# Performance work log

Measured on AMD Instinct MI355X. Metric: run time of the kernel, lower is better.

The kernel has to match this reference:

```python
import jax, jax.numpy as jnp
import numpy as np

N = 129  # fixed by fc1: 3*121 -> N-8 = 121
F = 262144
E = 16384

def setup_inputs() -> dict:
    key = jax.random.key(0)
    ks = jax.random.split(key, 18)
    s = 0.05
    return {
        "x": jax.random.normal(ks[0], (N, F), jnp.float32),
        "edge_index": jax.random.randint(ks[1], (2, E), 0, N),
        "edge_attr": jax.random.uniform(ks[2], (E, 3), jnp.float32),
        # GCNConvSortPool (channel1 only; forward reuses it for all 3 edge channels)
        "gcn1_W": jax.random.normal(ks[3], (F, 1), jnp.float32) * (1.0 / np.sqrt(F)),
        "gcn1_b": jnp.zeros((1,), jnp.float32),
        "gcn2_W": jax.random.normal(ks[4], (1, 1), jnp.float32),
        "gcn2_b": jnp.zeros((1,), jnp.float32),
        "conv1_w": jax.random.normal(ks[5], (3, 2, 3), jnp.float32) * s,  # OIH
        "conv1_b": jax.random.normal(ks[6], (3,), jnp.float32) * s,
        "conv2_w": jax.random.normal(ks[7], (1, 3, 3), jnp.float32) * s,
        "conv2_b": jax.random.normal(ks[8], (1,), jnp.float32) * s,
        "fc1_W": jax.random.normal(ks[9], (3 * 121, 32), jnp.float32) * s,
        "fc1_b": jnp.zeros((32,), jnp.float32),
        "fc2_W": jax.random.normal(ks[10], (32, 6), jnp.float32) * s,
        "fc2_b": jnp.zeros((6,), jnp.float32),
        "fc3_W": jax.random.normal(ks[11], (6, 2), jnp.float32) * s,
        "fc3_b": jnp.zeros((2,), jnp.float32),
    }

def _gcn_conv(x, row, col, ew, W, b):
    # PyG GCNConv with edge weights: add self loops (weight 1), symmetric norm.
    n = x.shape[0]
    xw = x @ W                                             # [n, out]
    loop = jnp.arange(n)
    row2 = jnp.concatenate([row, loop])
    col2 = jnp.concatenate([col, loop])
    ew2 = jnp.concatenate([ew, jnp.ones((n,), x.dtype)])
    deg = jax.ops.segment_sum(ew2, col2, num_segments=n)
    dinv = jnp.where(deg > 0, deg ** -0.5, 0.0)
    norm = dinv[row2] * ew2 * dinv[col2]                   # [e+n]
    out = jax.ops.segment_sum(norm[:, None] * xw[row2], col2, num_segments=n)
    return out + b

def _maxpool1d3(z):
    return jax.lax.reduce_window(z, -jnp.inf, jax.lax.max, (1, 1, 3), (1, 1, 1), 'VALID')

def _conv1d(z, w, b):
    out = jax.lax.conv_general_dilated(z, w, (1,), 'VALID', dimension_numbers=('NCH', 'OIH', 'NCH'))
    return out + b[None, :, None]

def _channel(x, row, col, ew, gcn1_W, gcn1_b, gcn2_W, gcn2_b, conv1_w, conv1_b, conv2_w, conv2_b):
    h1 = _gcn_conv(x, row, col, ew, gcn1_W, gcn1_b)        # [N,1]
    h2 = _gcn_conv(h1[:, -1:], row, col, ew, gcn2_W, gcn2_b)  # [N,1]
    h = jnp.concatenate([h1, h2], axis=-1)                 # [N,2]
    perm = jnp.argsort(-h[:, -1])                          # SortPool: sort by last channel, descending, k=N
    h = h[perm]                                            # [N,2]
    z = h.T[None]                                          # [1,2,N]
    z = _maxpool1d3(_conv1d(z, conv1_w, conv1_b))          # [1,3,N-4]
    z = _maxpool1d3(_conv1d(z, conv2_w, conv2_b))          # [1,1,N-8]
    return z

def reference(x, edge_index, edge_attr, gcn1_W, gcn1_b, gcn2_W, gcn2_b,
              conv1_w, conv1_b, conv2_w, conv2_b,
              fc1_W, fc1_b, fc2_W, fc2_b, fc3_W, fc3_b):
    row, col = edge_index[0], edge_index[1]
    outs = [_channel(x, row, col, edge_attr[:, c], gcn1_W, gcn1_b, gcn2_W, gcn2_b,
                     conv1_w, conv1_b, conv2_w, conv2_b) for c in range(3)]
    all_x = jnp.concatenate(outs, axis=-2)                 # [1,3,121]
    h = all_x.reshape(1, -1)                               # [1,363]
    h = jax.nn.elu(h @ fc1_W + fc1_b)                      # dropout=0 -> identity
    h = jax.nn.elu(h @ fc2_W + fc2_b)
    return h @ fc3_W + fc3_b                               # [1,2]
```

## Files before the change

kernel.cpp:

```cpp
#include <hip/hip_runtime.h>
#include <hip/hip_bf16.h>
#include <math.h>

#define NN 129
#define FF 262144
#define EE 16384
#define CHUNKS 32
#define CHUNK (FF / CHUNKS)
#define NMV (NN * CHUNKS)

#define EPT_T (EE / 256)
#define BATCH 8
#define NBATCH (EPT_T / BATCH)

#define OFF_PARTIAL 0
#define OFF_BAR     (OFF_PARTIAL + NMV)
#define OFF_SORT    (OFF_BAR + 1024)
#define LSTRIDE 32

typedef float vfloat4 __attribute__((ext_vector_type(4)));

__global__ __launch_bounds__(256) void k_fused(
    const float* __restrict__ x, const float* __restrict__ W,
    const int* __restrict__ eidx, const float* __restrict__ eattr,
    double* __restrict__ ws,
    const float* __restrict__ b1, const float* __restrict__ W2, const float* __restrict__ b2,
    const float* __restrict__ c1w, const float* __restrict__ c1b,
    const float* __restrict__ c2w, const float* __restrict__ c2b,
    const float* __restrict__ f1W, const float* __restrict__ f1b,
    const float* __restrict__ f2W, const float* __restrict__ f2b,
    const float* __restrict__ f3W, const float* __restrict__ f3b,
    float* __restrict__ out)
{
    const int b = blockIdx.x;
    const int tid = threadIdx.x;
    const int wave = tid >> 6, lane = tid & 63;

    __shared__ double P[129 + 387 + 387];
    __shared__ double SCR[1935];
    __shared__ int    sbin[NN];
    __shared__ int    scur[NN];
    __shared__ double ws4[4];
    __shared__ double fcb[38];

    unsigned* sync = (unsigned*)(ws + OFF_BAR);

    if (b != 0) {
        const int bm = b - 1;
        const int r = bm / CHUNKS, ch = bm % CHUNKS;
        const vfloat4* xp = (const vfloat4*)(x + (size_t)r * FF + (size_t)ch * CHUNK);
        const float4*  wp = (const float4*)(W + (size_t)ch * CHUNK);
        double acc0 = 0.0, acc1 = 0.0;
#pragma unroll
        for (int i = 0; i < CHUNK / (256 * 4); ++i) {
            vfloat4 xv = __builtin_nontemporal_load(xp + tid + i * 256);
            float4  wv = wp[tid + i * 256];
            acc0 += (double)xv[0] * (double)wv.x + (double)xv[1] * (double)wv.y;
            acc1 += (double)xv[2] * (double)wv.z + (double)xv[3] * (double)wv.w;
        }
        double acc = acc0 + acc1;
        for (int off = 32; off > 0; off >>= 1) acc += __shfl_down(acc, off, 64);
        if (lane == 0) ws4[wave] = acc;
        __syncthreads();
        if (tid == 0) {
            const double v = (ws4[0] + ws4[1]) + (ws4[2] + ws4[3]);
            __hip_atomic_store(&ws[OFF_PARTIAL + bm], v,
                               __ATOMIC_RELAXED, __HIP_MEMORY_SCOPE_AGENT);
            asm volatile("s_waitcnt vmcnt(0)" ::: "memory");
            __hip_atomic_fetch_add(&sync[(bm & 63) * LSTRIDE], 1u,
                                   __ATOMIC_RELAXED, __HIP_MEMORY_SCOPE_AGENT);
        }
        return;
    }

    double* sxw   = P;
    double* sdinv = P + 129;
    double* sh1   = P + 516;
    double* agg   = SCR;
    float4* recs  = (float4*)(ws + OFF_SORT);

    for (int i = tid; i < NN; i += 256) sbin[i] = 0;
    __syncthreads();
    for (int bt = 0; bt < NBATCH; ++bt) {
        int c8[BATCH];
#pragma unroll
        for (int i = 0; i < BATCH; ++i)
            c8[i] = eidx[EE + (bt * BATCH + i) * 256 + tid];
#pragma unroll
        for (int i = 0; i < BATCH; ++i) atomicAdd(&sbin[c8[i]], 1);
    }
    __syncthreads();
    if (tid == 0) {
        int run = 0;
        for (int j = 0; j < NN; ++j) { scur[j] = run; run += sbin[j]; }
    }
    __syncthreads();
    for (int bt = 0; bt < NBATCH; ++bt) {
        int r8[BATCH], c8[BATCH];
        float a8[BATCH][3];
#pragma unroll
        for (int i = 0; i < BATCH; ++i) {
            const int e = (bt * BATCH + i) * 256 + tid;
            r8[i] = eidx[e];
            c8[i] = eidx[EE + e];
            a8[i][0] = eattr[e * 3 + 0];
            a8[i][1] = eattr[e * 3 + 1];
            a8[i][2] = eattr[e * 3 + 2];
        }
#pragma unroll
        for (int i = 0; i < BATCH; ++i) {
            const int pos = atomicAdd(&scur[c8[i]], 1);
            float4 rec;
            rec.x = __int_as_float((r8[i] << 8) | c8[i]);
            rec.y = a8[i][0]; rec.z = a8[i][1]; rec.w = a8[i][2];
            recs[pos] = rec;
        }
    }
    __threadfence_block();
    __syncthreads();

    for (int i = tid; i < 3 * NN; i += 256) agg[i] = 0.0;
    __syncthreads();
    {
        const int base = tid * EPT_T;
        double a0 = 0.0, a1 = 0.0, a2 = 0.0;
        int cur = -1;
#pragma unroll 4
        for (int k = 0; k < EPT_T; ++k) {
            const float4 rec = recs[base + k];
            const int rc = __float_as_int(rec.x);
            const int cl = rc & 255;
            if (cl != cur) {
                if (cur >= 0) {
                    unsafeAtomicAdd(&agg[0 * NN + cur], a0);
                    unsafeAtomicAdd(&agg[1 * NN + cur], a1);
                    unsafeAtomicAdd(&agg[2 * NN + cur], a2);
                }
                cur = cl; a0 = a1 = a2 = 0.0;
            }
            a0 += (double)rec.y; a1 += (double)rec.z; a2 += (double)rec.w;
        }
        if (cur >= 0) {
            unsafeAtomicAdd(&agg[0 * NN + cur], a0);
            unsafeAtomicAdd(&agg[1 * NN + cur], a1);
            unsafeAtomicAdd(&agg[2 * NN + cur], a2);
        }
    }
    __syncthreads();
    for (int v = tid; v < 3 * NN; v += 256) {
        const double d = 1.0 + agg[v];
        sdinv[v] = (d > 0.0) ? 1.0 / sqrt(d) : 0.0;
    }
    __syncthreads();

    if (tid < 64) {
        unsigned* c = sync + tid * LSTRIDE;
        const unsigned expct = (tid < 32) ? 65u : 64u;
        while (__hip_atomic_load(c, __ATOMIC_RELAXED, __HIP_MEMORY_SCOPE_AGENT) < expct)
            __builtin_amdgcn_s_sleep(8);
    }
    __syncthreads();

    for (int j = tid; j < NN; j += 256) {
        double s = 0.0;
#pragma unroll
        for (int k = 0; k < CHUNKS; ++k)
            s += __hip_atomic_load(&ws[OFF_PARTIAL + j * CHUNKS + k],
                                   __ATOMIC_RELAXED, __HIP_MEMORY_SCOPE_AGENT);
        sxw[j] = s;
    }
    for (int i = tid; i < 3 * NN; i += 256) agg[i] = 0.0;
    __syncthreads();

    {
        const int base = tid * EPT_T;
        double a0 = 0.0, a1 = 0.0, a2 = 0.0;
        int cur = -1;
#pragma unroll 4
        for (int k = 0; k < EPT_T; ++k) {
            const float4 rec = recs[base + k];
            const int rc = __float_as_int(rec.x);
            const int cl = rc & 255, r = rc >> 8;
            if (cl != cur) {
                if (cur >= 0) {
                    unsafeAtomicAdd(&agg[0 * NN + cur], a0);
                    unsafeAtomicAdd(&agg[1 * NN + cur], a1);
                    unsafeAtomicAdd(&agg[2 * NN + cur], a2);
                }
                cur = cl; a0 = a1 = a2 = 0.0;
            }
            const double xwr = sxw[r];
            const double nw0 = sdinv[0 * NN + r] * (double)rec.y * sdinv[0 * NN + cl];
            const double nw1 = sdinv[1 * NN + r] * (double)rec.z * sdinv[1 * NN + cl];
            const double nw2 = sdinv[2 * NN + r] * (double)rec.w * sdinv[2 * NN + cl];
            a0 += nw0 * xwr; a1 += nw1 * xwr; a2 += nw2 * xwr;
        }
        if (cur >= 0) {
            unsafeAtomicAdd(&agg[0 * NN + cur], a0);
            unsafeAtomicAdd(&agg[1 * NN + cur], a1);
            unsafeAtomicAdd(&agg[2 * NN + cur], a2);
        }
    }
    __syncthreads();

    const double bb1 = (double)b1[0];
    for (int i = tid; i < 3 * NN; i += 256) {
        const int j = i % NN;
        const double dv = sdinv[i];
        sh1[i] = dv * dv * sxw[j] + bb1 + agg[i];
    }
    __syncthreads();
    for (int i = tid; i < 3 * NN; i += 256) agg[i] = 0.0;
    __syncthreads();

    const double w2 = (double)W2[0];
    {
        const int base = tid * EPT_T;
        double a0 = 0.0, a1 = 0.0, a2 = 0.0;
        int cur = -1;
#pragma unroll 4
        for (int k = 0; k < EPT_T; ++k) {
            const float4 rec = recs[base + k];
            const int rc = __float_as_int(rec.x);
            const int cl = rc & 255, r = rc >> 8;
            if (cl != cur) {
                if (cur >= 0) {
                    unsafeAtomicAdd(&agg[0 * NN + cur], a0);
                    unsafeAtomicAdd(&agg[1 * NN + cur], a1);
                    unsafeAtomicAdd(&agg[2 * NN + cur], a2);
                }
                cur = cl; a0 = a1 = a2 = 0.0;
            }
            const double nw0 = sdinv[0 * NN + r] * (double)rec.y * sdinv[0 * NN + cl];
            const double nw1 = sdinv[1 * NN + r] * (double)rec.z * sdinv[1 * NN + cl];
            const double nw2 = sdinv[2 * NN + r] * (double)rec.w * sdinv[2 * NN + cl];
            a0 += nw0 * (sh1[0 * NN + r] * w2);
            a1 += nw1 * (sh1[1 * NN + r] * w2);
            a2 += nw2 * (sh1[2 * NN + r] * w2);
        }
        if (cur >= 0) {
            unsafeAtomicAdd(&agg[0 * NN + cur], a0);
            unsafeAtomicAdd(&agg[1 * NN + cur], a1);
            unsafeAtomicAdd(&agg[2 * NN + cur], a2);
        }
    }
    __syncthreads();

    double* h2f = SCR + 1548;
    const double bb2 = (double)b2[0];
    for (int i = tid; i < 3 * NN; i += 256) {
        const int j = i % NN; (void)j;
        const double dv = sdinv[i];
        h2f[i] = dv * dv * (sh1[i] * w2) + bb2 + agg[i];
    }
    __syncthreads();

    double* z0   = SCR;
    double* z1   = SCR + 387;
    int*    rnk  = (int*)(SCR + 774);
    double* c1o  = SCR + 774;
    double* c2o  = SCR;
    double* allx = SCR + 369;
    double* fc1o = fcb;
    double* fc2o = fcb + 32;

    for (int i = tid; i < 3 * NN; i += 256) {
        const int c = i / NN, j = i % NN;
        const double v = h2f[c * NN + j];
        int rk = 0;
        for (int q = 0; q < NN; ++q) {
            const double u = h2f[c * NN + q];
            rk += (u > v) || (u == v && q < j);
        }
        rnk[i] = rk;
    }
    __syncthreads();
    for (int i = tid; i < 3 * NN; i += 256) {
        const int c = i / NN;
        const int rk = rnk[i];
        z0[c * NN + rk] = sh1[i];
        z1[c * NN + rk] = h2f[i];
    }
    __syncthreads();

    for (int i = tid; i < 3 * 3 * 127; i += 256) {
        const int c = i / (3 * 127), rem = i % (3 * 127), o = rem / 127, p = rem % 127;
        double s = (double)c1b[o];
#pragma unroll
        for (int k = 0; k < 3; ++k) {
            s += (double)c1w[(o * 2 + 0) * 3 + k] * z0[c * NN + p + k];
            s += (double)c1w[(o * 2 + 1) * 3 + k] * z1[c * NN + p + k];
        }
        c1o[(c * 3 + o) * 127 + p] = s;
    }
    __syncthreads();

    for (int i = tid; i < 3 * 123; i += 256) {
        const int c = i / 123, p = i % 123;
        double s = (double)c2b[0];
#pragma unroll
        for (int ic = 0; ic < 3; ++ic)
#pragma unroll
            for (int k = 0; k < 3; ++k) {
                const double* base = c1o + (c * 3 + ic) * 127 + p + k;
                const double m = fmax(base[0], fmax(base[1], base[2]));
                s += (double)c2w[ic * 3 + k] * m;
            }
        c2o[c * 123 + p] = s;
    }
    __syncthreads();
    for (int i = tid; i < 3 * 121; i += 256) {
        const int c = i / 121, p = i % 121;
        allx[c * 121 + p] = fmax(c2o[c * 123 + p],
                            fmax(c2o[c * 123 + p + 1], c2o[c * 123 + p + 2]));
    }
    __syncthreads();

    {
        const int j = tid >> 3, t = tid & 7;
        double s = 0.0;
        for (int i = t; i < 363; i += 8) s += allx[i] * (double)f1W[i * 32 + j];
        s += __shfl_down(s, 4, 8);
        s += __shfl_down(s, 2, 8);
        s += __shfl_down(s, 1, 8);
        if (t == 0) {
            s += (double)f1b[j];
            fc1o[j] = (s > 0.0) ? s : expm1(s);
        }
    }
    __syncthreads();
    if (tid < 6) {
        double s = (double)f2b[tid];
        for (int i = 0; i < 32; ++i) s += fc1o[i] * (double)f2W[i * 6 + tid];
        fc2o[tid] = (s > 0.0) ? s : expm1(s);
    }
    __syncthreads();
    if (tid < 2) {
        double s = (double)f3b[tid];
        for (int i = 0; i < 6; ++i) s += fc2o[i] * (double)f3W[i * 2 + tid];
        out[tid] = (float)s;
    }
}

extern "C" void kernel_launch(void* const* d_in, const int* in_sizes, int n_in,
                              void* d_out, int out_size, void* d_ws, size_t ws_size,
                              hipStream_t stream) {
    const float* x    = (const float*)d_in[0];
    const int*   eidx = (const int*)d_in[1];
    const float* eattr= (const float*)d_in[2];
    const float* g1W  = (const float*)d_in[3];
    const float* g1b  = (const float*)d_in[4];
    const float* g2W  = (const float*)d_in[5];
    const float* g2b  = (const float*)d_in[6];
    const float* c1w  = (const float*)d_in[7];
    const float* c1b  = (const float*)d_in[8];
    const float* c2w  = (const float*)d_in[9];
    const float* c2b  = (const float*)d_in[10];
    const float* f1W  = (const float*)d_in[11];
    const float* f1b  = (const float*)d_in[12];
    const float* f2W  = (const float*)d_in[13];
    const float* f2b  = (const float*)d_in[14];
    const float* f3W  = (const float*)d_in[15];
    const float* f3b  = (const float*)d_in[16];
    float* out = (float*)d_out;
    double* ws = (double*)d_ws;

    hipMemsetAsync((void*)(ws + OFF_BAR), 0, 64 * 128, stream);
    k_fused<<<NMV + 1, 256, 0, stream>>>(
        x, g1W, eidx, eattr, ws,
        g1b, g2W, g2b, c1w, c1b, c2w, c2b,
        f1W, f1b, f2W, f2b, f3W, f3b, out);
}
```

Before: 303.8 us.

## Drop per-launch memset by self-resetting device-global sync counters; batch edge scans

Replaces the workspace-based barrier counters, which were zeroed by a hipMemsetAsync before every launch, with a __device__ global array that block 0 resets to zero at the end of the kernel. This removes one extra GPU operation per call. The three edge-scan loops are factored into a templated helper that loads 8 records at a time, the partial-sum gather is batched, the scatter batch shrinks from 8 to 4, and launch bounds now request 6 blocks per SM. Correctness across calls now depends on every launch finishing its reset; an aborted run would leave stale counters.

```diff
diff --git a/kernel.cpp b/kernel.cpp
--- a/kernel.cpp
+++ b/kernel.cpp
@@ -1,5 +1,4 @@
 #include <hip/hip_runtime.h>
-#include <hip/hip_bf16.h>
 #include <math.h>
 
 #define NN 129
@@ -10,17 +9,74 @@
 #define NMV (NN * CHUNKS)
 
 #define EPT_T (EE / 256)
-#define BATCH 8
-#define NBATCH (EPT_T / BATCH)
+#define SB 8
+#define NSB (EPT_T / SB)
 
 #define OFF_PARTIAL 0
-#define OFF_BAR     (OFF_PARTIAL + NMV)
-#define OFF_SORT    (OFF_BAR + 1024)
+#define OFF_SORT    (OFF_PARTIAL + NMV)
+
 #define LSTRIDE 32
+__device__ __align__(128) unsigned g_sync[64 * LSTRIDE];
 
 typedef float vfloat4 __attribute__((ext_vector_type(4)));
 
-__global__ __launch_bounds__(256) void k_fused(
+__device__ __forceinline__ double agent_ld(const double* p) {
+    return __hip_atomic_load(p, __ATOMIC_RELAXED, __HIP_MEMORY_SCOPE_AGENT);
+}
+__device__ __forceinline__ void agent_st(double* p, double v) {
+    __hip_atomic_store(p, v, __ATOMIC_RELAXED, __HIP_MEMORY_SCOPE_AGENT);
+}
+
+template<int MODE>
+__device__ __forceinline__ void scan_edges(
+    const float4* __restrict__ recs, double* agg,
+    const double* sdinv, const double* sxw, const double* sh1,
+    double w2, int tid)
+{
+    const int base = tid * EPT_T;
+    double a0 = 0.0, a1 = 0.0, a2 = 0.0;
+    int cur = -1;
+    for (int bt = 0; bt < NSB; ++bt) {
+        float4 rb[SB];
+#pragma unroll
+        for (int i = 0; i < SB; ++i) rb[i] = recs[base + bt * SB + i];
+#pragma unroll
+        for (int i = 0; i < SB; ++i) {
+            const int rc = __float_as_int(rb[i].x);
+            const int cl = rc & 255, r = rc >> 8;
+            if (cl != cur) {
+                if (cur >= 0) {
+                    unsafeAtomicAdd(&agg[0 * NN + cur], a0);
+                    unsafeAtomicAdd(&agg[1 * NN + cur], a1);
+                    unsafeAtomicAdd(&agg[2 * NN + cur], a2);
+                }
+                cur = cl; a0 = a1 = a2 = 0.0;
+            }
+            if (MODE == 0) {
+                a0 += (double)rb[i].y; a1 += (double)rb[i].z; a2 += (double)rb[i].w;
+            } else {
+                const double nw0 = sdinv[0 * NN + r] * (double)rb[i].y * sdinv[0 * NN + cl];
+                const double nw1 = sdinv[1 * NN + r] * (double)rb[i].z * sdinv[1 * NN + cl];
+                const double nw2 = sdinv[2 * NN + r] * (double)rb[i].w * sdinv[2 * NN + cl];
+                if (MODE == 1) {
+                    const double xwr = sxw[r];
+                    a0 += nw0 * xwr; a1 += nw1 * xwr; a2 += nw2 * xwr;
+                } else {
+                    a0 += nw0 * (sh1[0 * NN + r] * w2);
+                    a1 += nw1 * (sh1[1 * NN + r] * w2);
+                    a2 += nw2 * (sh1[2 * NN + r] * w2);
+                }
+            }
+        }
+    }
+    if (cur >= 0) {
+        unsafeAtomicAdd(&agg[0 * NN + cur], a0);
+        unsafeAtomicAdd(&agg[1 * NN + cur], a1);
+        unsafeAtomicAdd(&agg[2 * NN + cur], a2);
+    }
+}
+
+__global__ __launch_bounds__(256, 6) void k_fused(
     const float* __restrict__ x, const float* __restrict__ W,
     const int* __restrict__ eidx, const float* __restrict__ eattr,
     double* __restrict__ ws,
@@ -43,8 +99,6 @@
     __shared__ double ws4[4];
     __shared__ double fcb[38];
 
-    unsigned* sync = (unsigned*)(ws + OFF_BAR);
-
     if (b != 0) {
         const int bm = b - 1;
         const int r = bm / CHUNKS, ch = bm % CHUNKS;
@@ -64,10 +118,9 @@
         __syncthreads();
         if (tid == 0) {
             const double v = (ws4[0] + ws4[1]) + (ws4[2] + ws4[3]);
-            __hip_atomic_store(&ws[OFF_PARTIAL + bm], v,
-                               __ATOMIC_RELAXED, __HIP_MEMORY_SCOPE_AGENT);
+            agent_st(&ws[OFF_PARTIAL + bm], v);
             asm volatile("s_waitcnt vmcnt(0)" ::: "memory");
-            __hip_atomic_fetch_add(&sync[(bm & 63) * LSTRIDE], 1u,
+            __hip_atomic_fetch_add(&g_sync[(bm & 63) * LSTRIDE], 1u,
                                    __ATOMIC_RELAXED, __HIP_MEMORY_SCOPE_AGENT);
         }
         return;
@@ -81,13 +134,13 @@
 
     for (int i = tid; i < NN; i += 256) sbin[i] = 0;
     __syncthreads();
-    for (int bt = 0; bt < NBATCH; ++bt) {
-        int c8[BATCH];
-#pragma unroll
-        for (int i = 0; i < BATCH; ++i)
-            c8[i] = eidx[EE + (bt * BATCH + i) * 256 + tid];
-#pragma unroll
-        for (int i = 0; i < BATCH; ++i) atomicAdd(&sbin[c8[i]], 1);
+    for (int bt = 0; bt < EPT_T / 8; ++bt) {
+        int c8[8];
+#pragma unroll
+        for (int i = 0; i < 8; ++i)
+            c8[i] = eidx[EE + (bt * 8 + i) * 256 + tid];
+#pragma unroll
+        for (int i = 0; i < 8; ++i) atomicAdd(&sbin[c8[i]], 1);
     }
     __syncthreads();
     if (tid == 0) {
@@ -95,24 +148,24 @@
         for (int j = 0; j < NN; ++j) { scur[j] = run; run += sbin[j]; }
     }
     __syncthreads();
-    for (int bt = 0; bt < NBATCH; ++bt) {
-        int r8[BATCH], c8[BATCH];
-        float a8[BATCH][3];
-#pragma unroll
-        for (int i = 0; i < BATCH; ++i) {
-            const int e = (bt * BATCH + i) * 256 + tid;
-            r8[i] = eidx[e];
-            c8[i] = eidx[EE + e];
-            a8[i][0] = eattr[e * 3 + 0];
-            a8[i][1] = eattr[e * 3 + 1];
-            a8[i][2] = eattr[e * 3 + 2];
-        }
-#pragma unroll
-        for (int i = 0; i < BATCH; ++i) {
-            const int pos = atomicAdd(&scur[c8[i]], 1);
+    for (int bt = 0; bt < EPT_T / 4; ++bt) {
+        int r4[4], c4[4];
+        float a4[4][3];
+#pragma unroll
+        for (int i = 0; i < 4; ++i) {
+            const int e = (bt * 4 + i) * 256 + tid;
+            r4[i] = eidx[e];
+            c4[i] = eidx[EE + e];
+            a4[i][0] = eattr[e * 3 + 0];
+            a4[i][1] = eattr[e * 3 + 1];
+            a4[i][2] = eattr[e * 3 + 2];
+        }
+#pragma unroll
+        for (int i = 0; i < 4; ++i) {
+            const int pos = atomicAdd(&scur[c4[i]], 1);
             float4 rec;
-            rec.x = __int_as_float((r8[i] << 8) | c8[i]);
-            rec.y = a8[i][0]; rec.z = a8[i][1]; rec.w = a8[i][2];
+            rec.x = __int_as_float((r4[i] << 8) | c4[i]);
+            rec.y = a4[i][0]; rec.z = a4[i][1]; rec.w = a4[i][2];
             recs[pos] = rec;
         }
     }
@@ -121,31 +174,7 @@
 
     for (int i = tid; i < 3 * NN; i += 256) agg[i] = 0.0;
     __syncthreads();
-    {
-        const int base = tid * EPT_T;
-        double a0 = 0.0, a1 = 0.0, a2 = 0.0;
-        int cur = -1;
-#pragma unroll 4
-        for (int k = 0; k < EPT_T; ++k) {
-            const float4 rec = recs[base + k];
-            const int rc = __float_as_int(rec.x);
-            const int cl = rc & 255;
-            if (cl != cur) {
-                if (cur >= 0) {
-                    unsafeAtomicAdd(&agg[0 * NN + cur], a0);
-                    unsafeAtomicAdd(&agg[1 * NN + cur], a1);
-                    unsafeAtomicAdd(&agg[2 * NN + cur], a2);
-                }
-                cur = cl; a0 = a1 = a2 = 0.0;
-            }
-            a0 += (double)rec.y; a1 += (double)rec.z; a2 += (double)rec.w;
-        }
-        if (cur >= 0) {
-            unsafeAtomicAdd(&agg[0 * NN + cur], a0);
-            unsafeAtomicAdd(&agg[1 * NN + cur], a1);
-            unsafeAtomicAdd(&agg[2 * NN + cur], a2);
-        }
-    }
+    scan_edges<0>(recs, agg, sdinv, sxw, sh1, 0.0, tid);
     __syncthreads();
     for (int v = tid; v < 3 * NN; v += 256) {
         const double d = 1.0 + agg[v];
@@ -154,7 +183,7 @@
     __syncthreads();
 
     if (tid < 64) {
-        unsigned* c = sync + tid * LSTRIDE;
+        unsigned* c = &g_sync[tid * LSTRIDE];
         const unsigned expct = (tid < 32) ? 65u : 64u;
         while (__hip_atomic_load(c, __ATOMIC_RELAXED, __HIP_MEMORY_SCOPE_AGENT) < expct)
             __builtin_amdgcn_s_sleep(8);
@@ -163,44 +192,20 @@
 
     for (int j = tid; j < NN; j += 256) {
         double s = 0.0;
-#pragma unroll
-        for (int k = 0; k < CHUNKS; ++k)
-            s += __hip_atomic_load(&ws[OFF_PARTIAL + j * CHUNKS + k],
-                                   __ATOMIC_RELAXED, __HIP_MEMORY_SCOPE_AGENT);
+        for (int kk = 0; kk < CHUNKS / 8; ++kk) {
+            double v8[8];
+#pragma unroll
+            for (int u = 0; u < 8; ++u)
+                v8[u] = agent_ld(&ws[OFF_PARTIAL + j * CHUNKS + kk * 8 + u]);
+#pragma unroll
+            for (int u = 0; u < 8; ++u) s += v8[u];
+        }
         sxw[j] = s;
     }
     for (int i = tid; i < 3 * NN; i += 256) agg[i] = 0.0;
     __syncthreads();
 
-    {
-        const int base = tid * EPT_T;
-        double a0 = 0.0, a1 = 0.0, a2 = 0.0;
-        int cur = -1;
-#pragma unroll 4
-        for (int k = 0; k < EPT_T; ++k) {
-            const float4 rec = recs[base + k];
-            const int rc = __float_as_int(rec.x);
-            const int cl = rc & 255, r = rc >> 8;
-            if (cl != cur) {
-                if (cur >= 0) {
-                    unsafeAtomicAdd(&agg[0 * NN + cur], a0);
-                    unsafeAtomicAdd(&agg[1 * NN + cur], a1);
-                    unsafeAtomicAdd(&agg[2 * NN + cur], a2);
-                }
-                cur = cl; a0 = a1 = a2 = 0.0;
-            }
-            const double xwr = sxw[r];
-            const double nw0 = sdinv[0 * NN + r] * (double)rec.y * sdinv[0 * NN + cl];
-            const double nw1 = sdinv[1 * NN + r] * (double)rec.z * sdinv[1 * NN + cl];
-            const double nw2 = sdinv[2 * NN + r] * (double)rec.w * sdinv[2 * NN + cl];
-            a0 += nw0 * xwr; a1 += nw1 * xwr; a2 += nw2 * xwr;
-        }
-        if (cur >= 0) {
-            unsafeAtomicAdd(&agg[0 * NN + cur], a0);
-            unsafeAtomicAdd(&agg[1 * NN + cur], a1);
-            unsafeAtomicAdd(&agg[2 * NN + cur], a2);
-        }
-    }
+    scan_edges<1>(recs, agg, sdinv, sxw, sh1, 0.0, tid);
     __syncthreads();
 
     const double bb1 = (double)b1[0];
@@ -214,42 +219,12 @@
     __syncthreads();
 
     const double w2 = (double)W2[0];
-    {
-        const int base = tid * EPT_T;
-        double a0 = 0.0, a1 = 0.0, a2 = 0.0;
-        int cur = -1;
-#pragma unroll 4
-        for (int k = 0; k < EPT_T; ++k) {
-            const float4 rec = recs[base + k];
-            const int rc = __float_as_int(rec.x);
-            const int cl = rc & 255, r = rc >> 8;
-            if (cl != cur) {
-                if (cur >= 0) {
-                    unsafeAtomicAdd(&agg[0 * NN + cur], a0);
-                    unsafeAtomicAdd(&agg[1 * NN + cur], a1);
-                    unsafeAtomicAdd(&agg[2 * NN + cur], a2);
-                }
-                cur = cl; a0 = a1 = a2 = 0.0;
-            }
-            const double nw0 = sdinv[0 * NN + r] * (double)rec.y * sdinv[0 * NN + cl];
-            const double nw1 = sdinv[1 * NN + r] * (double)rec.z * sdinv[1 * NN + cl];
-            const double nw2 = sdinv[2 * NN + r] * (double)rec.w * sdinv[2 * NN + cl];
-            a0 += nw0 * (sh1[0 * NN + r] * w2);
-            a1 += nw1 * (sh1[1 * NN + r] * w2);
-            a2 += nw2 * (sh1[2 * NN + r] * w2);
-        }
-        if (cur >= 0) {
-            unsafeAtomicAdd(&agg[0 * NN + cur], a0);
-            unsafeAtomicAdd(&agg[1 * NN + cur], a1);
-            unsafeAtomicAdd(&agg[2 * NN + cur], a2);
-        }
-    }
+    scan_edges<2>(recs, agg, sdinv, sxw, sh1, w2, tid);
     __syncthreads();
 
     double* h2f = SCR + 1548;
     const double bb2 = (double)b2[0];
     for (int i = tid; i < 3 * NN; i += 256) {
-        const int j = i % NN; (void)j;
         const double dv = sdinv[i];
         h2f[i] = dv * dv * (sh1[i] * w2) + bb2 + agg[i];
     }
@@ -340,6 +315,11 @@
         for (int i = 0; i < 6; ++i) s += fc2o[i] * (double)f3W[i * 2 + tid];
         out[tid] = (float)s;
     }
+
+    __syncthreads();
+    if (tid < 64)
+        __hip_atomic_store(&g_sync[tid * LSTRIDE], 0u,
+                           __ATOMIC_RELAXED, __HIP_MEMORY_SCOPE_AGENT);
 }
 
 extern "C" void kernel_launch(void* const* d_in, const int* in_sizes, int n_in,
@@ -365,7 +345,6 @@
     float* out = (float*)d_out;
     double* ws = (double*)d_ws;
 
-    hipMemsetAsync((void*)(ws + OFF_BAR), 0, 64 * 128, stream);
     k_fused<<<NMV + 1, 256, 0, stream>>>(
         x, g1W, eidx, eattr, ws,
         g1b, g2W, g2b, c1w, c1b, c2w, c2b,
```

Result: faster. 297.3 us (-2.2%).
